# Optimization experiments

Hardware: AMD Instinct MI355X
Metric: run time of the kernel (lower is better)

## Reference

```python
import jax, jax.numpy as jnp
import numpy as np

NUM_SYMBOLS = 100000
EMBED_DIM = 256
DIM = 2 * EMBED_DIM          # 512
NUM_HEADS = 4
HEAD_DIM = DIM // NUM_HEADS  # 128
N = 100                      # hard-coded neighbor count in source
EPS = 1e-5


def layernorm(x, g, b):
    mu = jnp.mean(x, axis=-1, keepdims=True)
    var = jnp.var(x, axis=-1, keepdims=True)
    return (x - mu) * jax.lax.rsqrt(var + EPS) * g + b


def setup_inputs() -> dict:
    key = jax.random.key(0)
    ks = jax.random.split(key, 12)
    B, FEW = 512, 2
    connections = jax.random.randint(ks[0], (B, FEW, N, 2), 0, NUM_SYMBOLS)
    mask = jax.random.randint(ks[1], (B * FEW, N, N), 0, 2).astype(jnp.int32)
    s = 0.02
    emb = jax.random.normal(ks[2], (NUM_SYMBOLS + 1, EMBED_DIM), jnp.float32) * s
    qkv_w = jax.random.normal(ks[3], (3 * DIM, DIM), jnp.float32) * s
    qkv_b = jnp.zeros((3 * DIM,), jnp.float32)
    proj_w = jax.random.normal(ks[4], (DIM, DIM), jnp.float32) * s
    proj_b = jnp.zeros((DIM,), jnp.float32)
    ln1_g = jnp.ones((DIM,), jnp.float32); ln1_b = jnp.zeros((DIM,), jnp.float32)
    ln2_g = jnp.ones((DIM,), jnp.float32); ln2_b = jnp.zeros((DIM,), jnp.float32)
    fc_w = jax.random.normal(ks[5], (DIM // 2, DIM), jnp.float32) * s
    fc_b = jnp.zeros((DIM // 2,), jnp.float32)
    return {"connections": connections, "mask": mask, "emb": emb,
            "qkv_w": qkv_w, "qkv_b": qkv_b, "proj_w": proj_w, "proj_b": proj_b,
            "ln1_g": ln1_g, "ln1_b": ln1_b, "ln2_g": ln2_g, "ln2_b": ln2_b,
            "fc_w": fc_w, "fc_b": fc_b}


def reference(connections, mask, emb, qkv_w, qkv_b, proj_w, proj_b,
              ln1_g, ln1_b, ln2_g, ln2_b, fc_w, fc_b):
    # embedding gathers for (relation, entity) pairs
    rel = emb[connections[..., 0]]          # [B, few, N, E]
    ent = emb[connections[..., 1]]          # [B, few, N, E]
    x = jnp.concatenate([rel, ent], axis=-1).reshape(-1, N, DIM)  # [BN, N, C]
    m = mask.reshape(-1, N, N)

    xn = layernorm(x, ln1_g, ln1_b)
    qkv = xn @ qkv_w.T + qkv_b              # [BN, N, 3C]
    BN = xn.shape[0]
    qkv = qkv.reshape(BN, N, 3, NUM_HEADS, HEAD_DIM).transpose(2, 0, 3, 1, 4)
    q, k, v = qkv[0], qkv[1], qkv[2]        # [BN, H, N, hd]

    scale = HEAD_DIM ** -0.5
    attn = jnp.einsum('bhnd,bhmd->bhnm', q, k) * scale
    attn = jnp.where(m[:, None] == 0, -1e9, attn)
    attn = jax.nn.softmax(attn, axis=-1)    # [BN, H, N, N]

    y = jnp.einsum('bhnm,bhmd->bhnd', attn, v)
    y = y.transpose(0, 2, 1, 3).reshape(BN, N, DIM)
    y = y @ proj_w.T + proj_b               # [BN, N, C]

    # attn.mean(dim=2): mean over query axis -> [BN, H, N]; bmm with y
    wc = jnp.einsum('bhn,bnc->bhc', attn.mean(axis=2), y)   # [BN, H, C]
    out = layernorm(wc, ln2_g, ln2_b) @ fc_w.T + fc_b       # [BN, H, C//2]
    return out
```

## Files before the change

### kernel.cpp

```cpp
#include <hip/hip_runtime.h>
#include <stdint.h>

typedef __attribute__((ext_vector_type(8))) short bf16x8;
typedef __attribute__((ext_vector_type(4))) float f32x4;
typedef __attribute__((ext_vector_type(4))) unsigned int u32x4;
typedef __attribute__((ext_vector_type(4))) unsigned short u16x4;

typedef const void __attribute__((address_space(1))) gvoid_t;
typedef void __attribute__((address_space(3))) lvoid_t;

__device__ __forceinline__ unsigned short f2bf(float f) {
  union { float f; unsigned int u; } v; v.f = f;
  unsigned int u = v.u;
  u += 0x7fffu + ((u >> 16) & 1u);
  return (unsigned short)(u >> 16);
}
__device__ __forceinline__ float bf2f(unsigned short h) {
  union { unsigned int u; float f; } v; v.u = ((unsigned int)h) << 16;
  return v.f;
}
__device__ __forceinline__ void load_lds16(const void* g, void* l) {
  __builtin_amdgcn_global_load_lds((gvoid_t*)g, (lvoid_t*)l, 16, 0, 0);
}

#define GATE4() asm volatile("s_waitcnt vmcnt(4)" ::: "memory")
#define GATE0() asm volatile("s_waitcnt vmcnt(0)" ::: "memory")
#define BARRIER()                    \
  do {                               \
    asm volatile("" ::: "memory");   \
    __builtin_amdgcn_s_barrier();    \
    asm volatile("" ::: "memory");   \
  } while (0)

__global__ __launch_bounds__(256) void k_prep(const float* __restrict__ s0, int n0,
                                              const float* __restrict__ s1, int n1,
                                              const float* __restrict__ s2, int n2,
                                              unsigned short* __restrict__ d0,
                                              unsigned short* __restrict__ d1,
                                              unsigned short* __restrict__ d2,
                                              const int* __restrict__ mask,
                                              unsigned int* __restrict__ bm,
                                              int ncvtblk) {
  if ((int)blockIdx.x < ncvtblk) {
    int i = blockIdx.x * 256 + threadIdx.x;
    if (i < n0) { d0[i] = f2bf(s0[i]); return; }
    i -= n0;
    if (i < n1) { d1[i] = f2bf(s1[i]); return; }
    i -= n1;
    if (i < n2) d2[i] = f2bf(s2[i]);
    return;
  }
  const int lane = threadIdx.x & 63;
  const int wv = ((blockIdx.x - ncvtblk) << 2) + (threadIdx.x >> 6);
  const int r0 = wv * 16;
  for (int i = 0; i < 16; ++i) {
    const int r = r0 + i;
    const size_t base = (size_t)r * 100;
    const int c0 = mask[base + lane];
    int c1 = 0;
    if (lane < 36) c1 = mask[base + 64 + lane];
    const unsigned long long b0 = __ballot(c0 != 0);
    const unsigned long long b1 = __ballot(c1 != 0);
    if (lane == 0) {
      u32x4 v;
      v[0] = (unsigned int)b0; v[1] = (unsigned int)(b0 >> 32);
      v[2] = (unsigned int)b1; v[3] = (unsigned int)(b1 >> 32);
      *(u32x4*)(bm + (size_t)r * 4) = v;
    }
  }
}

__global__ __launch_bounds__(256) void k_gather_ln(const int* __restrict__ conn,
                                                   const float* __restrict__ emb,
                                                   const float* __restrict__ g1,
                                                   const float* __restrict__ b1,
                                                   unsigned short* __restrict__ xn,
                                                   int row0) {
  const int lane = threadIdx.x & 63;
  const int wid = threadIdx.x >> 6;
  const int rloc = blockIdx.x * 4 + wid;
  const int row = row0 + rloc;
  const int rel = conn[row * 2 + 0];
  const int ent = conn[row * 2 + 1];
  const float4 r4 = *(const float4*)(emb + (size_t)rel * 256 + lane * 4);
  const float4 e4 = *(const float4*)(emb + (size_t)ent * 256 + lane * 4);
  float rv[4] = {r4.x, r4.y, r4.z, r4.w};
  float ev[4] = {e4.x, e4.y, e4.z, e4.w};
  float s = 0.f, ss = 0.f;
#pragma unroll
  for (int j = 0; j < 4; ++j) { s += rv[j] + ev[j]; ss += rv[j] * rv[j] + ev[j] * ev[j]; }
#pragma unroll
  for (int d = 1; d < 64; d <<= 1) { s += __shfl_xor(s, d, 64); ss += __shfl_xor(ss, d, 64); }
  const float mu = s * (1.f / 512.f);
  const float var = ss * (1.f / 512.f) - mu * mu;
  const float rs = rsqrtf(var + 1e-5f);
  const float4 ga = *(const float4*)(g1 + lane * 4);
  const float4 gb = *(const float4*)(g1 + 256 + lane * 4);
  const float4 ba = *(const float4*)(b1 + lane * 4);
  const float4 bb = *(const float4*)(b1 + 256 + lane * 4);
  float gav[4] = {ga.x, ga.y, ga.z, ga.w}, gbv[4] = {gb.x, gb.y, gb.z, gb.w};
  float bav[4] = {ba.x, ba.y, ba.z, ba.w}, bbv[4] = {bb.x, bb.y, bb.z, bb.w};
  u16x4 o0, o1;
#pragma unroll
  for (int j = 0; j < 4; ++j) {
    o0[j] = f2bf((rv[j] - mu) * rs * gav[j] + bav[j]);
    o1[j] = f2bf((ev[j] - mu) * rs * gbv[j] + bbv[j]);
  }
  unsigned short* orow = xn + (size_t)rloc * 512;
  *(u16x4*)(orow + lane * 4) = o0;
  *(u16x4*)(orow + 256 + lane * 4) = o1;
}

template <typename CT>
__global__ __launch_bounds__(256) void k_gemm3(const unsigned short* __restrict__ A,
                                               const unsigned short* __restrict__ W,
                                               const float* __restrict__ bias,
                                               CT* __restrict__ C,
                                               int N, int K, int ntiles, int nwg) {
  __shared__ __align__(16) unsigned short ldsA[3][128 * 32];
  __shared__ __align__(16) unsigned short ldsB[3][128 * 32];

  const int orig = blockIdx.x;
  const int q = nwg >> 3, r = nwg & 7;
  const int xcd = orig & 7, idx = orig >> 3;
  const int wg = (xcd < r ? xcd * (q + 1) : r * (q + 1) + (xcd - r) * q) + idx;
  const int mtile = wg / ntiles, ntile = wg % ntiles;

  const int t = threadIdx.x, lane = t & 63, wid = t >> 6;
  const int wm = wid >> 1, wn = wid & 1;
  const size_t Abase = (size_t)mtile * 128 * K;
  const size_t Wbase = (size_t)ntile * 128 * K;
  const int NT = K >> 5;

  f32x4 acc[4][4];
#pragma unroll
  for (int i = 0; i < 4; ++i)
#pragma unroll
    for (int j = 0; j < 4; ++j) acc[i][j] = (f32x4){0.f, 0.f, 0.f, 0.f};

  const int sr0 = t >> 2;
  auto stage = [&](int buf, int kt) {
#pragma unroll
    for (int it = 0; it < 2; ++it) {
      const int row = it * 64 + sr0;
      const int cl = (t & 3) ^ ((row >> 1) & 3);
      load_lds16(A + Abase + (size_t)row * K + kt * 32 + cl * 8, &ldsA[buf][it * 2048 + t * 8]);
    }
#pragma unroll
    for (int it = 0; it < 2; ++it) {
      const int row = it * 64 + sr0;
      const int cl = (t & 3) ^ ((row >> 1) & 3);
      load_lds16(W + Wbase + (size_t)row * K + kt * 32 + cl * 8, &ldsB[buf][it * 2048 + t * 8]);
    }
  };

  stage(0, 0);
  stage(1, 1);

  int cur = 0;
  for (int kt = 0; kt < NT; ++kt) {
    if (kt + 1 < NT) { GATE4(); } else { GATE0(); }
    BARRIER();
    if (kt + 2 < NT) {
      int s2 = cur + 2; if (s2 >= 3) s2 -= 3;
      stage(s2, kt + 2);
    }
    bf16x8 af[4], bfr[4];
#pragma unroll
    for (int mi = 0; mi < 4; ++mi) {
      const int row = wm * 64 + mi * 16 + (lane & 15);
      const int st = (lane >> 4) ^ ((row >> 1) & 3);
      af[mi] = *(const bf16x8*)&ldsA[cur][row * 32 + st * 8];
    }
#pragma unroll
    for (int ni = 0; ni < 4; ++ni) {
      const int row = wn * 64 + ni * 16 + (lane & 15);
      const int st = (lane >> 4) ^ ((row >> 1) & 3);
      bfr[ni] = *(const bf16x8*)&ldsB[cur][row * 32 + st * 8];
    }
#pragma unroll
    for (int mi = 0; mi < 4; ++mi)
#pragma unroll
      for (int ni = 0; ni < 4; ++ni)
        acc[mi][ni] = __builtin_amdgcn_mfma_f32_16x16x32_bf16(af[mi], bfr[ni], acc[mi][ni], 0, 0, 0);
    cur = (cur + 1 == 3) ? 0 : cur + 1;
  }

#pragma unroll
  for (int ni = 0; ni < 4; ++ni) {
    const int col = ntile * 128 + wn * 64 + ni * 16 + (lane & 15);
    const float bv = bias[col];
#pragma unroll
    for (int mi = 0; mi < 4; ++mi) {
      const int row0 = mtile * 128 + wm * 64 + mi * 16 + ((lane >> 4) << 2);
#pragma unroll
      for (int r2 = 0; r2 < 4; ++r2) {
        const float ov = acc[mi][ni][r2] + bv;
        if constexpr (sizeof(CT) == 2)
          C[(size_t)(row0 + r2) * N + col] = (CT)f2bf(ov);
        else
          C[(size_t)(row0 + r2) * N + col] = (CT)ov;
      }
    }
  }
}

__global__ __launch_bounds__(512) void k_attn(const unsigned short* __restrict__ qkv,
                                              const unsigned int* __restrict__ bm,
                                              unsigned short* __restrict__ y,
                                              float* __restrict__ am, int b0) {
  __shared__ __align__(16) unsigned short A_lds[128 * 128];
  __shared__ __align__(16) unsigned short P_lds[7 * 16 * 128];
  __shared__ float am_s[112];
  const int t = threadIdx.x, lane = t & 63, w = t >> 6;
  const int bl = blockIdx.x >> 2, h = blockIdx.x & 3;
  const int bg = b0 + bl;
  const unsigned short* qk = qkv + (size_t)bl * 153600;

  if (t < 112) am_s[t] = 0.f;

#pragma unroll
  for (int j = 0; j < 4; ++j) {
    const int row = j * 32 + w * 4 + (lane >> 4);
    if (row < 100) {
      const int c = (lane & 15) ^ (row & 7);
      load_lds16(qk + (size_t)row * 1536 + 512 + h * 128 + c * 8,
                 &A_lds[j * 4096 + w * 512 + lane * 8]);
    }
  }
  u32x4 vv[4];
#pragma unroll
  for (int p = 0; p < 4; ++p) {
    const int vm = p * 32 + (t >> 4);
    const u32x4 z = {0u, 0u, 0u, 0u};
    vv[p] = (vm < 100) ? *(const u32x4*)(qk + (size_t)vm * 1536 + 1024 + h * 128 + (t & 15) * 8) : z;
  }
  bf16x8 qf[4];
  {
    const int qrow = w * 16 + (lane & 15);
    const bool qv = (w < 7) && (qrow < 100);
#pragma unroll
    for (int kk = 0; kk < 4; ++kk) {
      const bf16x8 z = {0, 0, 0, 0, 0, 0, 0, 0};
      qf[kk] = qv ? *(const bf16x8*)(qk + (size_t)qrow * 1536 + h * 128 + kk * 32 + (lane >> 4) * 8) : z;
    }
  }
  if (t < 192) {
    const u32x4 z = {0u, 0u, 0u, 0u};
    *(u32x4*)&A_lds[(100 + (t >> 4)) * 128 + (t & 15) * 8] = z;
  }
  __syncthreads();

  f32x4 sa[7];
#pragma unroll
  for (int ni = 0; ni < 7; ++ni) sa[ni] = (f32x4){0.f, 0.f, 0.f, 0.f};
  if (w < 7) {
#pragma unroll
    for (int kk = 0; kk < 4; ++kk)
#pragma unroll
      for (int ni = 0; ni < 7; ++ni) {
        const int row = ni * 16 + (lane & 15);
        const int c = (kk * 4 + (lane >> 4)) ^ (row & 7);
        const bf16x8 kf = *(const bf16x8*)&A_lds[row * 128 + (c << 3)];
        sa[ni] = __builtin_amdgcn_mfma_f32_16x16x32_bf16(qf[kk], kf, sa[ni], 0, 0, 0);
      }
  }
  __syncthreads();

#pragma unroll
  for (int p = 0; p < 4; ++p) {
    const int vm = p * 32 + (t >> 4);
    unsigned short tmp[8];
    *(u32x4*)tmp = vv[p];
#pragma unroll
    for (int jj = 0; jj < 8; ++jj) {
      const int d = (lane & 15) * 8 + jj;
      const int swz = (vm >> 3) ^ (((d >> 3) ^ d) & 7);
      A_lds[d * 128 + swz * 8 + (vm & 7)] = tmp[jj];
    }
  }

  if (w < 7) {
    const float scale = 0.08838834764831843f;
    float psum[7] = {0.f, 0.f, 0.f, 0.f, 0.f, 0.f, 0.f};
#pragma unroll
    for (int r = 0; r < 4; ++r) {
      const int lr = (lane >> 4) * 4 + r;
      const int qrow = w * 16 + lr;
      if (qrow < 100) {
        const u32x4 bmv = *(const u32x4*)(bm + ((size_t)bg * 100 + qrow) * 4);
        float x[7];
#pragma unroll
        for (int ni = 0; ni < 7; ++ni) {
          const int col = ni * 16 + (lane & 15);
          const unsigned int bit = (bmv[ni >> 1] >> (((ni & 1) << 4) + (lane & 15))) & 1u;
          x[ni] = (col < 100) ? (bit ? sa[ni][r] * scale : -1e9f) : -1e30f;
        }
        float mx = x[0];
#pragma unroll
        for (int ni = 1; ni < 7; ++ni) mx = fmaxf(mx, x[ni]);
#pragma unroll
        for (int dd = 1; dd < 16; dd <<= 1) mx = fmaxf(mx, __shfl_xor(mx, dd, 64));
        float e[7], sum = 0.f;
#pragma unroll
        for (int ni = 0; ni < 7; ++ni) { e[ni] = __expf(x[ni] - mx); sum += e[ni]; }
#pragma unroll
        for (int dd = 1; dd < 16; dd <<= 1) sum += __shfl_xor(sum, dd, 64);
        const float inv = 1.f / sum;
#pragma unroll
        for (int ni = 0; ni < 7; ++ni) {
          const float pv = e[ni] * inv;
          psum[ni] += pv;
          const int col = ni * 16 + (lane & 15);
          const int c = (col >> 3) ^ (lr & 7);
          P_lds[w * 2048 + lr * 128 + c * 8 + (col & 7)] = f2bf(pv);
        }
      } else {
#pragma unroll
        for (int ni = 0; ni < 7; ++ni) {
          const int col = ni * 16 + (lane & 15);
          const int c = (col >> 3) ^ (lr & 7);
          P_lds[w * 2048 + lr * 128 + c * 8 + (col & 7)] = 0;
        }
      }
    }
    if (lane < 32) {
      const int lr = lane & 15;
      const int c = (14 + (lane >> 4)) ^ (lr & 7);
      const u32x4 z = {0u, 0u, 0u, 0u};
      *(u32x4*)&P_lds[w * 2048 + lr * 128 + c * 8] = z;
    }
#pragma unroll
    for (int ni = 0; ni < 7; ++ni) atomicAdd(&am_s[ni * 16 + (lane & 15)], psum[ni]);
  }
  __syncthreads();

  if (t < 100) am[((size_t)bg * 4 + h) * 100 + t] = am_s[t] * 0.01f;

  if (w < 7) {
#pragma unroll
    for (int dt = 0; dt < 8; ++dt) {
      f32x4 acc = {0.f, 0.f, 0.f, 0.f};
#pragma unroll
      for (int kk = 0; kk < 4; ++kk) {
        const int c = kk * 4 + (lane >> 4);
        const bf16x8 pf = *(const bf16x8*)&P_lds[w * 2048 + (lane & 15) * 128 + ((c ^ (lane & 7)) << 3)];
        const int d = dt * 16 + (lane & 15);
        const int cv = c ^ (((d >> 3) ^ d) & 7);
        const bf16x8 vf = *(const bf16x8*)&A_lds[d * 128 + (cv << 3)];
        acc = __builtin_amdgcn_mfma_f32_16x16x32_bf16(pf, vf, acc, 0, 0, 0);
      }
      const int d = dt * 16 + (lane & 15);
#pragma unroll
      for (int r = 0; r < 4; ++r) {
        const int qrow = w * 16 + (lane >> 4) * 4 + r;
        if (qrow < 100)
          y[((size_t)bl * 100 + qrow) * 512 + h * 128 + d] = f2bf(acc[r]);
      }
    }
  }
}

__global__ __launch_bounds__(256) void k_z(const float* __restrict__ am,
                                           const unsigned short* __restrict__ y,
                                           unsigned short* __restrict__ zb, int b0) {
  __shared__ float ams[400];
  const int bl = blockIdx.x, t = threadIdx.x;
  const int bg = b0 + bl;
  for (int i = t; i < 400; i += 256) ams[i] = am[(size_t)bg * 400 + i];
  __syncthreads();
  float a0[4] = {0, 0, 0, 0}, a1[4] = {0, 0, 0, 0};
  const unsigned short* yb = y + (size_t)bl * 100 * 512 + t * 2;
#pragma unroll 4
  for (int n = 0; n < 100; ++n) {
    const unsigned int u = *(const unsigned int*)(yb + (size_t)n * 512);
    const float v0 = bf2f((unsigned short)(u & 0xffffu));
    const float v1 = bf2f((unsigned short)(u >> 16));
#pragma unroll
    for (int hh = 0; hh < 4; ++hh) {
      const float ww = ams[hh * 100 + n];
      a0[hh] += ww * v0;
      a1[hh] += ww * v1;
    }
  }
#pragma unroll
  for (int hh = 0; hh < 4; ++hh) {
    const unsigned int pk = (unsigned int)f2bf(a0[hh]) | ((unsigned int)f2bf(a1[hh]) << 16);
    *(unsigned int*)(zb + ((size_t)(bl * 4 + hh)) * 512 + 2 * t) = pk;
  }
}

__global__ __launch_bounds__(256) void k_ln2(const unsigned short* __restrict__ wcb,
                                             const float* __restrict__ g2,
                                             const float* __restrict__ b2,
                                             unsigned short* __restrict__ wcn) {
  const int t = threadIdx.x, lane = t & 63, w = t >> 6;
  const int row = blockIdx.x * 4 + w;
  const u32x4 pv = *(const u32x4*)(wcb + (size_t)row * 512 + lane * 8);
  float v[8];
#pragma unroll
  for (int j = 0; j < 4; ++j) {
    v[2 * j] = bf2f((unsigned short)(pv[j] & 0xffffu));
    v[2 * j + 1] = bf2f((unsigned short)(pv[j] >> 16));
  }
  float s = 0.f, ss = 0.f;
#pragma unroll
  for (int j = 0; j < 8; ++j) { s += v[j]; ss += v[j] * v[j]; }
#pragma unroll
  for (int d = 1; d < 64; d <<= 1) { s += __shfl_xor(s, d, 64); ss += __shfl_xor(ss, d, 64); }
  const float mu = s * (1.f / 512.f);
  const float var = ss * (1.f / 512.f) - mu * mu;
  const float rs = rsqrtf(var + 1e-5f);
  const float4 ga = *(const float4*)(g2 + lane * 8);
  const float4 gb = *(const float4*)(g2 + lane * 8 + 4);
  const float4 ba = *(const float4*)(b2 + lane * 8);
  const float4 bb = *(const float4*)(b2 + lane * 8 + 4);
  const float gv[8] = {ga.x, ga.y, ga.z, ga.w, gb.x, gb.y, gb.z, gb.w};
  const float bv[8] = {ba.x, ba.y, ba.z, ba.w, bb.x, bb.y, bb.z, bb.w};
  u32x4 ov;
#pragma unroll
  for (int j = 0; j < 4; ++j) {
    const unsigned short lo = f2bf((v[2 * j] - mu) * rs * gv[2 * j] + bv[2 * j]);
    const unsigned short hi = f2bf((v[2 * j + 1] - mu) * rs * gv[2 * j + 1] + bv[2 * j + 1]);
    ov[j] = (unsigned int)lo | ((unsigned int)hi << 16);
  }
  *(u32x4*)(wcn + (size_t)row * 512 + lane * 8) = ov;
}

extern "C" void kernel_launch(void* const* d_in, const int* in_sizes, int n_in,
                              void* d_out, int out_size, void* d_ws, size_t ws_size,
                              hipStream_t stream) {
  const int* conn = (const int*)d_in[0];
  const int* mask = (const int*)d_in[1];
  const float* emb = (const float*)d_in[2];
  const float* qkv_w = (const float*)d_in[3];
  const float* qkv_b = (const float*)d_in[4];
  const float* proj_w = (const float*)d_in[5];
  const float* proj_b = (const float*)d_in[6];
  const float* ln1g = (const float*)d_in[7];
  const float* ln1b = (const float*)d_in[8];
  const float* ln2g = (const float*)d_in[9];
  const float* ln2b = (const float*)d_in[10];
  const float* fc_w = (const float*)d_in[11];
  const float* fc_b = (const float*)d_in[12];
  float* out = (float*)d_out;

  size_t off = 0;
  auto alloc = [&](size_t bytes) {
    void* p = (char*)d_ws + off;
    off += (bytes + 255) & ~(size_t)255;
    return p;
  };
  unsigned short* w_qkv = (unsigned short*)alloc((size_t)1536 * 512 * 2);
  unsigned short* w_proj = (unsigned short*)alloc((size_t)512 * 512 * 2);
  unsigned short* w_fc = (unsigned short*)alloc((size_t)256 * 512 * 2);
  float* am = (float*)alloc((size_t)1024 * 400 * 4);
  unsigned int* bmb = (unsigned int*)alloc((size_t)102400 * 16);
  const size_t fixed = off;

  int CB = 1024;
  while (CB > 64) {
    size_t need = fixed + (size_t)CB * 4 * 512 * 2 * 3 + (size_t)CB * 100 * 512 * 2 +
                  (size_t)CB * 100 * 1536 * 2 + 8192;
    if (need <= ws_size) break;
    CB >>= 1;
  }
  unsigned short* zbuf = (unsigned short*)alloc((size_t)CB * 4 * 512 * 2);
  unsigned short* wcb = (unsigned short*)alloc((size_t)CB * 4 * 512 * 2);
  unsigned short* wcn = (unsigned short*)alloc((size_t)CB * 4 * 512 * 2);
  unsigned short* xn = (unsigned short*)alloc((size_t)CB * 100 * 512 * 2);
  unsigned short* qkvb = (unsigned short*)alloc((size_t)CB * 100 * 1536 * 2);

  const int ncvtblk = (786432 + 262144 + 131072 + 255) / 256;
  k_prep<<<ncvtblk + 1600, 256, 0, stream>>>(qkv_w, 786432, proj_w, 262144, fc_w, 131072,
                                             w_qkv, w_proj, w_fc, mask, bmb, ncvtblk);

  for (int b0 = 0; b0 < 1024; b0 += CB) {
    const int mt = CB * 100 / 128;
    const int zt = CB * 4 / 128;
    k_gather_ln<<<CB * 25, 256, 0, stream>>>(conn, emb, ln1g, ln1b, xn, b0 * 100);
    k_gemm3<unsigned short><<<12 * mt, 256, 0, stream>>>(xn, w_qkv, qkv_b, qkvb, 1536, 512, 12, 12 * mt);
    k_attn<<<CB * 4, 512, 0, stream>>>(qkvb, bmb, xn , am, b0);
    k_z<<<CB, 256, 0, stream>>>(am, xn , zbuf, b0);
    k_gemm3<unsigned short><<<4 * zt, 256, 0, stream>>>(zbuf, w_proj, proj_b, wcb, 512, 512, 4, 4 * zt);
    k_ln2<<<CB, 256, 0, stream>>>(wcb, ln2g, ln2b, wcn);
    k_gemm3<float><<<2 * zt, 256, 0, stream>>>(wcn, w_fc, fc_b, out + (size_t)b0 * 1024, 256, 512, 2, 2 * zt);
  }
}
```

Before: 539.4 us.

## Fuse attention-weighted sum, projection, LayerNorm2 and FC into one kernel; vectorize GEMM epilogue

The separate z-reduction, projection GEMM, LN2 and FC GEMM kernels are replaced by one per-batch kernel. It keeps z and the normalized rows in shared memory and does the two small matvec-style products with scalar FMAs over bf16 weights. This removes three launches and their intermediate global round-trips, but the tail stages no longer use MFMA. The QKV GEMM also swaps its MFMA operand order, so each lane holds four consecutive columns and stores them as one packed 8-byte write instead of scattered 2-byte writes.

New measurement: 617.6 us. 1.15x slower.

```diff
diff --git a/kernel.cpp b/kernel.cpp
--- a/kernel.cpp
+++ b/kernel.cpp
@@ -111,11 +111,10 @@
   *(u16x4*)(orow + 256 + lane * 4) = o1;
 }
 
-template <typename CT>
 __global__ __launch_bounds__(256) void k_gemm3(const unsigned short* __restrict__ A,
                                                const unsigned short* __restrict__ W,
                                                const float* __restrict__ bias,
-                                               CT* __restrict__ C,
+                                               unsigned short* __restrict__ C,
                                                int N, int K, int ntiles, int nwg) {
   __shared__ __align__(16) unsigned short ldsA[3][128 * 32];
   __shared__ __align__(16) unsigned short ldsB[3][128 * 32];
@@ -182,25 +181,23 @@
     for (int mi = 0; mi < 4; ++mi)
 #pragma unroll
       for (int ni = 0; ni < 4; ++ni)
-        acc[mi][ni] = __builtin_amdgcn_mfma_f32_16x16x32_bf16(af[mi], bfr[ni], acc[mi][ni], 0, 0, 0);
+        acc[mi][ni] = __builtin_amdgcn_mfma_f32_16x16x32_bf16(bfr[ni], af[mi], acc[mi][ni], 0, 0, 0);
     cur = (cur + 1 == 3) ? 0 : cur + 1;
   }
 
 #pragma unroll
   for (int ni = 0; ni < 4; ++ni) {
-    const int col = ntile * 128 + wn * 64 + ni * 16 + (lane & 15);
-    const float bv = bias[col];
+    const int colb = ntile * 128 + wn * 64 + ni * 16 + ((lane >> 4) << 2);
+    const float4 bv = *(const float4*)(bias + colb);
 #pragma unroll
     for (int mi = 0; mi < 4; ++mi) {
-      const int row0 = mtile * 128 + wm * 64 + mi * 16 + ((lane >> 4) << 2);
-#pragma unroll
-      for (int r2 = 0; r2 < 4; ++r2) {
-        const float ov = acc[mi][ni][r2] + bv;
-        if constexpr (sizeof(CT) == 2)
-          C[(size_t)(row0 + r2) * N + col] = (CT)f2bf(ov);
-        else
-          C[(size_t)(row0 + r2) * N + col] = (CT)ov;
-      }
+      const int row = mtile * 128 + wm * 64 + mi * 16 + (lane & 15);
+      const unsigned int lo =
+          (unsigned int)f2bf(acc[mi][ni][0] + bv.x) | ((unsigned int)f2bf(acc[mi][ni][1] + bv.y) << 16);
+      const unsigned int hi =
+          (unsigned int)f2bf(acc[mi][ni][2] + bv.z) | ((unsigned int)f2bf(acc[mi][ni][3] + bv.w) << 16);
+      uint2 pk; pk.x = lo; pk.y = hi;
+      *(uint2*)(C + (size_t)row * N + colb) = pk;
     }
   }
 }
@@ -361,70 +358,105 @@
   }
 }
 
-__global__ __launch_bounds__(256) void k_z(const float* __restrict__ am,
-                                           const unsigned short* __restrict__ y,
-                                           unsigned short* __restrict__ zb, int b0) {
+__global__ __launch_bounds__(256) void k_final2(const float* __restrict__ am,
+                                                const unsigned short* __restrict__ y,
+                                                const unsigned short* __restrict__ wp,
+                                                const float* __restrict__ pb,
+                                                const float* __restrict__ g2,
+                                                const float* __restrict__ b2,
+                                                const unsigned short* __restrict__ fcw,
+                                                const float* __restrict__ fcb,
+                                                float* __restrict__ out, int b0) {
   __shared__ float ams[400];
+  __shared__ float z[4][512];
+  __shared__ float wcn[4][512];
   const int bl = blockIdx.x, t = threadIdx.x;
   const int bg = b0 + bl;
   for (int i = t; i < 400; i += 256) ams[i] = am[(size_t)bg * 400 + i];
   __syncthreads();
-  float a0[4] = {0, 0, 0, 0}, a1[4] = {0, 0, 0, 0};
-  const unsigned short* yb = y + (size_t)bl * 100 * 512 + t * 2;
+  {
+    float a0[4] = {0, 0, 0, 0}, a1[4] = {0, 0, 0, 0};
+    const unsigned short* yb = y + (size_t)bl * 100 * 512 + t * 2;
 #pragma unroll 4
-  for (int n = 0; n < 100; ++n) {
-    const unsigned int u = *(const unsigned int*)(yb + (size_t)n * 512);
-    const float v0 = bf2f((unsigned short)(u & 0xffffu));
-    const float v1 = bf2f((unsigned short)(u >> 16));
+    for (int n = 0; n < 100; ++n) {
+      const unsigned int u = *(const unsigned int*)(yb + (size_t)n * 512);
+      const float v0 = bf2f((unsigned short)(u & 0xffffu));
+      const float v1 = bf2f((unsigned short)(u >> 16));
+#pragma unroll
+      for (int hh = 0; hh < 4; ++hh) {
+        const float ww = ams[hh * 100 + n];
+        a0[hh] += ww * v0;
+        a1[hh] += ww * v1;
+      }
+    }
 #pragma unroll
     for (int hh = 0; hh < 4; ++hh) {
-      const float ww = ams[hh * 100 + n];
-      a0[hh] += ww * v0;
-      a1[hh] += ww * v1;
-    }
-  }
-#pragma unroll
-  for (int hh = 0; hh < 4; ++hh) {
-    const unsigned int pk = (unsigned int)f2bf(a0[hh]) | ((unsigned int)f2bf(a1[hh]) << 16);
-    *(unsigned int*)(zb + ((size_t)(bl * 4 + hh)) * 512 + 2 * t) = pk;
-  }
-}
-
-__global__ __launch_bounds__(256) void k_ln2(const unsigned short* __restrict__ wcb,
-                                             const float* __restrict__ g2,
-                                             const float* __restrict__ b2,
-                                             unsigned short* __restrict__ wcn) {
-  const int t = threadIdx.x, lane = t & 63, w = t >> 6;
-  const int row = blockIdx.x * 4 + w;
-  const u32x4 pv = *(const u32x4*)(wcb + (size_t)row * 512 + lane * 8);
-  float v[8];
-#pragma unroll
-  for (int j = 0; j < 4; ++j) {
-    v[2 * j] = bf2f((unsigned short)(pv[j] & 0xffffu));
-    v[2 * j + 1] = bf2f((unsigned short)(pv[j] >> 16));
-  }
-  float s = 0.f, ss = 0.f;
-#pragma unroll
-  for (int j = 0; j < 8; ++j) { s += v[j]; ss += v[j] * v[j]; }
-#pragma unroll
-  for (int d = 1; d < 64; d <<= 1) { s += __shfl_xor(s, d, 64); ss += __shfl_xor(ss, d, 64); }
-  const float mu = s * (1.f / 512.f);
-  const float var = ss * (1.f / 512.f) - mu * mu;
-  const float rs = rsqrtf(var + 1e-5f);
-  const float4 ga = *(const float4*)(g2 + lane * 8);
-  const float4 gb = *(const float4*)(g2 + lane * 8 + 4);
-  const float4 ba = *(const float4*)(b2 + lane * 8);
-  const float4 bb = *(const float4*)(b2 + lane * 8 + 4);
-  const float gv[8] = {ga.x, ga.y, ga.z, ga.w, gb.x, gb.y, gb.z, gb.w};
-  const float bv[8] = {ba.x, ba.y, ba.z, ba.w, bb.x, bb.y, bb.z, bb.w};
-  u32x4 ov;
-#pragma unroll
-  for (int j = 0; j < 4; ++j) {
-    const unsigned short lo = f2bf((v[2 * j] - mu) * rs * gv[2 * j] + bv[2 * j]);
-    const unsigned short hi = f2bf((v[2 * j + 1] - mu) * rs * gv[2 * j + 1] + bv[2 * j + 1]);
-    ov[j] = (unsigned int)lo | ((unsigned int)hi << 16);
-  }
-  *(u32x4*)(wcn + (size_t)row * 512 + lane * 8) = ov;
+      z[hh][2 * t] = a0[hh];
+      z[hh][2 * t + 1] = a1[hh];
+    }
+  }
+  __syncthreads();
+#pragma unroll
+  for (int cc = 0; cc < 2; ++cc) {
+    const int c = t + cc * 256;
+    const unsigned short* wr = wp + (size_t)c * 512;
+    float acc4[4] = {0, 0, 0, 0};
+    for (int k0 = 0; k0 < 512; k0 += 8) {
+      unsigned short w8[8];
+      *(u32x4*)w8 = *(const u32x4*)(wr + k0);
+#pragma unroll
+      for (int j = 0; j < 8; ++j) {
+        const float wv = bf2f(w8[j]);
+#pragma unroll
+        for (int hh = 0; hh < 4; ++hh) acc4[hh] += wv * z[hh][k0 + j];
+      }
+    }
+    const float pbv = pb[c];
+#pragma unroll
+    for (int hh = 0; hh < 4; ++hh) wcn[hh][c] = acc4[hh] + pbv;
+  }
+  __syncthreads();
+  {
+    const int hh = t >> 6, lane = t & 63;
+    float vals[8];
+    float s = 0.f, ss = 0.f;
+#pragma unroll
+    for (int j = 0; j < 8; ++j) {
+      const float v = wcn[hh][lane * 8 + j];
+      vals[j] = v;
+      s += v;
+      ss += v * v;
+    }
+#pragma unroll
+    for (int d = 1; d < 64; d <<= 1) { s += __shfl_xor(s, d, 64); ss += __shfl_xor(ss, d, 64); }
+    const float mu = s * (1.f / 512.f);
+    const float var = ss * (1.f / 512.f) - mu * mu;
+    const float rs = rsqrtf(var + 1e-5f);
+#pragma unroll
+    for (int j = 0; j < 8; ++j) {
+      const int c2 = lane * 8 + j;
+      wcn[hh][c2] = (vals[j] - mu) * rs * g2[c2] + b2[c2];
+    }
+  }
+  __syncthreads();
+  {
+    const int o = t;
+    const unsigned short* fr = fcw + (size_t)o * 512;
+    float acc4[4] = {0, 0, 0, 0};
+    for (int k0 = 0; k0 < 512; k0 += 8) {
+      unsigned short w8[8];
+      *(u32x4*)w8 = *(const u32x4*)(fr + k0);
+#pragma unroll
+      for (int j = 0; j < 8; ++j) {
+        const float wv = bf2f(w8[j]);
+#pragma unroll
+        for (int hh = 0; hh < 4; ++hh) acc4[hh] += wv * wcn[hh][k0 + j];
+      }
+    }
+    const float fb = fcb[o];
+#pragma unroll
+    for (int hh = 0; hh < 4; ++hh) out[(size_t)bg * 1024 + hh * 256 + o] = acc4[hh] + fb;
+  }
 }
 
 extern "C" void kernel_launch(void* const* d_in, const int* in_sizes, int n_in,
@@ -460,14 +492,10 @@
 
   int CB = 1024;
   while (CB > 64) {
-    size_t need = fixed + (size_t)CB * 4 * 512 * 2 * 3 + (size_t)CB * 100 * 512 * 2 +
-                  (size_t)CB * 100 * 1536 * 2 + 8192;
+    size_t need = fixed + (size_t)CB * 100 * 512 * 2 + (size_t)CB * 100 * 1536 * 2 + 8192;
     if (need <= ws_size) break;
     CB >>= 1;
   }
-  unsigned short* zbuf = (unsigned short*)alloc((size_t)CB * 4 * 512 * 2);
-  unsigned short* wcb = (unsigned short*)alloc((size_t)CB * 4 * 512 * 2);
-  unsigned short* wcn = (unsigned short*)alloc((size_t)CB * 4 * 512 * 2);
   unsigned short* xn = (unsigned short*)alloc((size_t)CB * 100 * 512 * 2);
   unsigned short* qkvb = (unsigned short*)alloc((size_t)CB * 100 * 1536 * 2);
 
@@ -477,13 +505,10 @@
 
   for (int b0 = 0; b0 < 1024; b0 += CB) {
     const int mt = CB * 100 / 128;
-    const int zt = CB * 4 / 128;
     k_gather_ln<<<CB * 25, 256, 0, stream>>>(conn, emb, ln1g, ln1b, xn, b0 * 100);
-    k_gemm3<unsigned short><<<12 * mt, 256, 0, stream>>>(xn, w_qkv, qkv_b, qkvb, 1536, 512, 12, 12 * mt);
+    k_gemm3<<<12 * mt, 256, 0, stream>>>(xn, w_qkv, qkv_b, qkvb, 1536, 512, 12, 12 * mt);
     k_attn<<<CB * 4, 512, 0, stream>>>(qkvb, bmb, xn , am, b0);
-    k_z<<<CB, 256, 0, stream>>>(am, xn , zbuf, b0);
-    k_gemm3<unsigned short><<<4 * zt, 256, 0, stream>>>(zbuf, w_proj, proj_b, wcb, 512, 512, 4, 4 * zt);
-    k_ln2<<<CB, 256, 0, stream>>>(wcb, ln2g, ln2b, wcn);
-    k_gemm3<float><<<2 * zt, 256, 0, stream>>>(wcn, w_fc, fc_b, out + (size_t)b0 * 1024, 256, 512, 2, 2 * zt);
-  }
-}
+    k_final2<<<CB, 256, 0, stream>>>(am, xn , w_proj, proj_b, ln2g, ln2b, w_fc, fc_b,
+                                     out, b0);
+  }
+}
```

## Load GEMM weight fragments directly into registers, bypassing LDS staging

Applied to the files above, without the earlier changes.

The GEMM kernel no longer stages the weight (B) tile through LDS. Each wave now loads its B fragments straight from global memory into registers, double-buffered one k-step ahead. The k-loop is unrolled by two to ping-pong the register buffers, and the vmcnt gate is raised to account for the extra in-flight loads. This removes B-side LDS writes and reads and halves shared memory use. In exchange, waves that share a B column block load it redundantly from global or L2, and the loop assumes an even number of k-tiles.

Result: slower. 677.2 us (+25.5%).

```diff
diff --git a/kernel.cpp b/kernel.cpp
--- a/kernel.cpp
+++ b/kernel.cpp
@@ -23,7 +23,7 @@
   __builtin_amdgcn_global_load_lds((gvoid_t*)g, (lvoid_t*)l, 16, 0, 0);
 }
 
-#define GATE4() asm volatile("s_waitcnt vmcnt(4)" ::: "memory")
+#define GATE6() asm volatile("s_waitcnt vmcnt(6)" ::: "memory")
 #define GATE0() asm volatile("s_waitcnt vmcnt(0)" ::: "memory")
 #define BARRIER()                    \
   do {                               \
@@ -111,6 +111,40 @@
   *(u16x4*)(orow + 256 + lane * 4) = o1;
 }
 
+#define LOADB(KT, DST)                                                                   \
+  do {                                                                                   \
+    _Pragma("unroll")                                                                    \
+    for (int ni = 0; ni < 4; ++ni)                                                       \
+      DST[ni] = *(const bf16x8*)(Wb + (size_t)(ni * 16 + (lane & 15)) * K + (KT) * 32 +  \
+                                 (lane >> 4) * 8);                                       \
+  } while (0)
+
+#define GSTEP(KT, BCUR, BNXT)                                                            \
+  do {                                                                                   \
+    if ((KT) + 1 < NT) { GATE6(); } else { GATE0(); }                                    \
+    BARRIER();                                                                           \
+    if ((KT) + 1 < NT) LOADB((KT) + 1, BNXT);                                            \
+    if ((KT) + 2 < NT) {                                                                 \
+      int s2 = cur + 2;                                                                  \
+      if (s2 >= 3) s2 -= 3;                                                              \
+      stageA(s2, (KT) + 2);                                                              \
+    }                                                                                    \
+    bf16x8 af[4];                                                                        \
+    _Pragma("unroll")                                                                    \
+    for (int mi = 0; mi < 4; ++mi) {                                                     \
+      const int row = wm * 64 + mi * 16 + (lane & 15);                                   \
+      const int st = (lane >> 4) ^ ((row >> 1) & 3);                                     \
+      af[mi] = *(const bf16x8*)&ldsA[cur][row * 32 + st * 8];                            \
+    }                                                                                    \
+    _Pragma("unroll")                                                                    \
+    for (int mi = 0; mi < 4; ++mi)                                                       \
+      _Pragma("unroll")                                                                  \
+      for (int ni = 0; ni < 4; ++ni)                                                     \
+        acc[mi][ni] =                                                                    \
+            __builtin_amdgcn_mfma_f32_16x16x32_bf16(af[mi], BCUR[ni], acc[mi][ni], 0, 0, 0); \
+    cur = (cur + 1 == 3) ? 0 : cur + 1;                                                  \
+  } while (0)
+
 template <typename CT>
 __global__ __launch_bounds__(256) void k_gemm3(const unsigned short* __restrict__ A,
                                                const unsigned short* __restrict__ W,
@@ -118,7 +152,6 @@
                                                CT* __restrict__ C,
                                                int N, int K, int ntiles, int nwg) {
   __shared__ __align__(16) unsigned short ldsA[3][128 * 32];
-  __shared__ __align__(16) unsigned short ldsB[3][128 * 32];
 
   const int orig = blockIdx.x;
   const int q = nwg >> 3, r = nwg & 7;
@@ -129,7 +162,7 @@
   const int t = threadIdx.x, lane = t & 63, wid = t >> 6;
   const int wm = wid >> 1, wn = wid & 1;
   const size_t Abase = (size_t)mtile * 128 * K;
-  const size_t Wbase = (size_t)ntile * 128 * K;
+  const unsigned short* Wb = W + (size_t)(ntile * 128 + wn * 64) * K;
   const int NT = K >> 5;
 
   f32x4 acc[4][4];
@@ -139,51 +172,24 @@
     for (int j = 0; j < 4; ++j) acc[i][j] = (f32x4){0.f, 0.f, 0.f, 0.f};
 
   const int sr0 = t >> 2;
-  auto stage = [&](int buf, int kt) {
+  auto stageA = [&](int buf, int kt) {
 #pragma unroll
     for (int it = 0; it < 2; ++it) {
       const int row = it * 64 + sr0;
       const int cl = (t & 3) ^ ((row >> 1) & 3);
       load_lds16(A + Abase + (size_t)row * K + kt * 32 + cl * 8, &ldsA[buf][it * 2048 + t * 8]);
     }
-#pragma unroll
-    for (int it = 0; it < 2; ++it) {
-      const int row = it * 64 + sr0;
-      const int cl = (t & 3) ^ ((row >> 1) & 3);
-      load_lds16(W + Wbase + (size_t)row * K + kt * 32 + cl * 8, &ldsB[buf][it * 2048 + t * 8]);
-    }
   };
 
-  stage(0, 0);
-  stage(1, 1);
+  stageA(0, 0);
+  stageA(1, 1);
+  bf16x8 bA[4], bB[4];
+  LOADB(0, bA);
 
   int cur = 0;
-  for (int kt = 0; kt < NT; ++kt) {
-    if (kt + 1 < NT) { GATE4(); } else { GATE0(); }
-    BARRIER();
-    if (kt + 2 < NT) {
-      int s2 = cur + 2; if (s2 >= 3) s2 -= 3;
-      stage(s2, kt + 2);
-    }
-    bf16x8 af[4], bfr[4];
-#pragma unroll
-    for (int mi = 0; mi < 4; ++mi) {
-      const int row = wm * 64 + mi * 16 + (lane & 15);
-      const int st = (lane >> 4) ^ ((row >> 1) & 3);
-      af[mi] = *(const bf16x8*)&ldsA[cur][row * 32 + st * 8];
-    }
-#pragma unroll
-    for (int ni = 0; ni < 4; ++ni) {
-      const int row = wn * 64 + ni * 16 + (lane & 15);
-      const int st = (lane >> 4) ^ ((row >> 1) & 3);
-      bfr[ni] = *(const bf16x8*)&ldsB[cur][row * 32 + st * 8];
-    }
-#pragma unroll
-    for (int mi = 0; mi < 4; ++mi)
-#pragma unroll
-      for (int ni = 0; ni < 4; ++ni)
-        acc[mi][ni] = __builtin_amdgcn_mfma_f32_16x16x32_bf16(af[mi], bfr[ni], acc[mi][ni], 0, 0, 0);
-    cur = (cur + 1 == 3) ? 0 : cur + 1;
+  for (int kt = 0; kt < NT; kt += 2) {
+    GSTEP(kt, bA, bB);
+    GSTEP(kt + 1, bB, bA);
   }
 
 #pragma unroll
```
